# Optimization experiments

Measured on AMD Instinct MI355X. Metric: run time of the kernel, lower is better.

## Reference

```python
import jax, jax.numpy as jnp
import numpy as np

EPS = 1e-5


def conv1x1(x, w, b=None):
    # x: [B,C,H,W], w: [O,C] (1x1 conv kernel squeezed)
    y = jnp.einsum('bchw,oc->bohw', x, w)
    if b is not None:
        y = y + b[None, :, None, None]
    return y


def bn_inf(x, g, b, m, v):
    scale = g / jnp.sqrt(v + EPS)
    return (x - m[None, :, None, None]) * scale[None, :, None, None] + b[None, :, None, None]


def setup_inputs() -> dict:
    B, C, H, W = 2, 256, 80, 80
    Ck, Cv, Co = 64, 128, 256
    key = jax.random.key(0)
    ks = jax.random.split(key, 16)
    d = {}
    d['x'] = jax.random.normal(ks[0], (B, C, H, W), dtype=jnp.float32)
    d['y'] = jax.random.normal(ks[1], (B, C, H, W), dtype=jnp.float32)
    s = 1.0 / np.sqrt(C)
    d['fk_w'] = jax.random.normal(ks[2], (Ck, C), dtype=jnp.float32) * s
    d['fk_g'] = jnp.ones((Ck,), jnp.float32)
    d['fk_b'] = jnp.zeros((Ck,), jnp.float32)
    d['fk_m'] = jax.random.normal(ks[3], (Ck,), dtype=jnp.float32) * 0.1
    d['fk_v'] = jax.random.uniform(ks[4], (Ck,), minval=0.5, maxval=1.5, dtype=jnp.float32)
    d['fq_w'] = jax.random.normal(ks[5], (Ck, C), dtype=jnp.float32) * s
    d['fq_g'] = jnp.ones((Ck,), jnp.float32)
    d['fq_b'] = jnp.zeros((Ck,), jnp.float32)
    d['fq_m'] = jax.random.normal(ks[6], (Ck,), dtype=jnp.float32) * 0.1
    d['fq_v'] = jax.random.uniform(ks[7], (Ck,), minval=0.5, maxval=1.5, dtype=jnp.float32)
    d['fv_w'] = jax.random.normal(ks[8], (Cv, C), dtype=jnp.float32) * s
    d['fv_b'] = jnp.zeros((Cv,), jnp.float32)
    d['W_w'] = jax.random.normal(ks[9], (Co, Cv), dtype=jnp.float32) * (1.0 / np.sqrt(Cv))
    d['W_b'] = jnp.zeros((Co,), jnp.float32)
    d['gamma'] = jnp.array([0.5], jnp.float32)
    return d


def reference(x, y, fk_w, fk_g, fk_b, fk_m, fk_v, fq_w, fq_g, fq_b, fq_m, fq_v, fv_w, fv_b, W_w, W_b, gamma):
    B, C, H, W = x.shape
    Ck = fk_w.shape[0]
    Cv = fv_w.shape[0]
    N = H * W
    # key from x, query/value from y (1x1 conv + BN projections)
    k = bn_inf(conv1x1(x, fk_w), fk_g, fk_b, fk_m, fk_v).reshape(B, Ck, N)          # [B,Ck,N]
    q = bn_inf(conv1x1(y, fq_w), fq_g, fq_b, fq_m, fq_v).reshape(B, Ck, N)          # [B,Ck,N]
    v = conv1x1(y, fv_w, fv_b).reshape(B, Cv, N)                                     # [B,Cv,N]
    sim = jnp.einsum('bkn,bkm->bnm', q, k) * (Ck ** -0.5)                            # [B,N,N]
    sim = jax.nn.softmax(sim, axis=-1)
    ctx = jnp.einsum('bnm,bvm->bvn', sim, v).reshape(B, Cv, H, W)                    # [B,Cv,H,W]
    ctx = conv1x1(ctx, W_w, W_b)                                                     # [B,Co,H,W]
    return gamma[0] * ctx + x
```

## Files before the change

kernel.cpp:

```cpp
#include <hip/hip_runtime.h>
#include <math.h>

#define NB   2
#define CIN  256
#define NN   6400
#define CKd  64
#define CVd  128
#define COd  256

using bf16   = __bf16;
using bf16x4 = __attribute__((ext_vector_type(4))) bf16;
using bf16x8 = __attribute__((ext_vector_type(8))) bf16;
using f32x4  = __attribute__((ext_vector_type(4))) float;

__device__ __forceinline__ void lds_cp16(const void* g, void* l) {
    __builtin_amdgcn_global_load_lds((const __attribute__((address_space(1))) void*)g,
                                     (__attribute__((address_space(3))) void*)l, 16, 0, 0);
}

__global__ void prep_kernel(const float* __restrict__ fk_w, const float* __restrict__ fk_g,
                            const float* __restrict__ fk_b, const float* __restrict__ fk_m,
                            const float* __restrict__ fk_v,
                            const float* __restrict__ fq_w, const float* __restrict__ fq_g,
                            const float* __restrict__ fq_b, const float* __restrict__ fq_m,
                            const float* __restrict__ fq_v,
                            const float* __restrict__ fv_w, const float* __restrict__ fv_b,
                            const float* __restrict__ W_w,  const float* __restrict__ W_b,
                            bf16* __restrict__ wkb, bf16* __restrict__ wqb,
                            bf16* __restrict__ wvb, bf16* __restrict__ wob,
                            float* __restrict__ bias)
{
    const int idx = blockIdx.x * 256 + threadIdx.x;
    const float QS = 0.18033688011112042f;
    if (idx < 16384) {
        const int co = idx >> 8;
        const float a = fk_g[co] * rsqrtf(fk_v[co] + 1e-5f);
        wkb[idx] = (bf16)(fk_w[idx] * a);
    } else if (idx < 32768) {
        const int i = idx - 16384, co = i >> 8;
        const float a = fq_g[co] * rsqrtf(fq_v[co] + 1e-5f) * QS;
        wqb[i] = (bf16)(fq_w[i] * a);
    } else if (idx < 65536) {
        const int i = idx - 32768;
        wvb[i] = (bf16)fv_w[i];
    } else if (idx < 98304) {
        const int i = idx - 65536;
        wob[i] = (bf16)W_w[i];
    } else if (idx < 98816) {
        const int j = idx - 98304;
        if (j < 64)       { const float a = fk_g[j] * rsqrtf(fk_v[j] + 1e-5f); bias[j] = fk_b[j] - fk_m[j] * a; }
        else if (j < 128) { const int c = j - 64; const float a = fq_g[c] * rsqrtf(fq_v[c] + 1e-5f); bias[j] = (fq_b[c] - fq_m[c] * a) * QS; }
        else if (j < 256) bias[j] = fv_b[j - 128];
        else              bias[j] = W_b[j - 256];
    }
}

__launch_bounds__(256, 2)
__global__ void projkqv_kernel(const float* __restrict__ x, const float* __restrict__ y,
                               const bf16* __restrict__ wkb, const bf16* __restrict__ wqb,
                               const bf16* __restrict__ wvb, const float* __restrict__ bias,
                               bf16* __restrict__ kb, bf16* __restrict__ qb, bf16* __restrict__ vb)
{
    __shared__ __align__(16) bf16 sbuf[64 * 256];
    __shared__ __align__(16) bf16 wbuf[64 * 256];

    const int tid  = threadIdx.x;
    const int lane = tid & 63, wav = tid >> 6;
    const int l15  = lane & 15, quad = lane >> 4;
    const int b    = blockIdx.z, m = blockIdx.y;
    const int n0   = blockIdx.x * 64;

    const float* srcg = ((m == 0) ? x : y) + (size_t)b * CIN * NN;
    const bf16* wg    = (m == 0) ? wkb : (m == 1) ? wqb : (wvb + (size_t)(m - 2) * 64 * CIN);

    {
        const int r2  = lane >> 5;
        const int c32 = lane & 31;
#pragma unroll
        for (int i = 0; i < 8; ++i) {
            const int rg = wav * 16 + i * 2;
            const int r  = rg + r2;
            const int cs = c32 ^ (r & 7);
            lds_cp16(wg + (size_t)r * 256 + cs * 8, &wbuf[rg * 256]);
        }
    }

    {
        const int cb = tid >> 4;
        const int nl = (tid & 15) * 4;
#pragma unroll
        for (int p = 0; p < 16; ++p) {
            const int c = cb + p * 16;
            const float4 v = *(const float4*)(srcg + (size_t)c * NN + n0 + nl);
            const int c16 = c >> 3, ce = c & 7;
#pragma unroll
            for (int i = 0; i < 4; ++i) {
                const int n = nl + i;
                sbuf[n * 256 + ((c16 ^ (n & 7)) << 3) + ce] = (bf16)(&v.x)[i];
            }
        }
    }
    __syncthreads();

    const int key = l15 & 7;
    f32x4 acc[4];
#pragma unroll
    for (int j = 0; j < 4; ++j) acc[j] = (f32x4){0.f, 0.f, 0.f, 0.f};

    if (m < 2) {
        const int arow = wav * 16 + l15;
#pragma unroll
        for (int k4 = 0; k4 < 32; k4 += 4) {
            const bf16x8 af = *(const bf16x8*)&sbuf[arow * 256 + ((k4 + quad) ^ key) * 8];
#pragma unroll
            for (int nt = 0; nt < 4; ++nt) {
                const int brow = nt * 16 + l15;
                const bf16x8 bfw = *(const bf16x8*)&wbuf[brow * 256 + ((k4 + quad) ^ key) * 8];
                acc[nt] = __builtin_amdgcn_mfma_f32_16x16x32_bf16(af, bfw, acc[nt], 0, 0, 0);
            }
        }
        const float* bs = bias + m * 64;
        bf16* dst = (m == 0) ? kb : qb;
        const int nb = n0 + wav * 16;
#pragma unroll
        for (int nt = 0; nt < 4; ++nt) {
            const float bv = bs[nt * 16 + l15];
#pragma unroll
            for (int r = 0; r < 4; ++r) {
                const int n = nb + quad * 4 + r;
                dst[((size_t)b * NN + n) * CKd + nt * 16 + l15] = (bf16)(acc[nt][r] + bv);
            }
        }
    } else {
        const int arow = wav * 16 + l15;
#pragma unroll
        for (int k4 = 0; k4 < 32; k4 += 4) {
            const bf16x8 af = *(const bf16x8*)&wbuf[arow * 256 + ((k4 + quad) ^ key) * 8];
#pragma unroll
            for (int nt = 0; nt < 4; ++nt) {
                const int brow = nt * 16 + l15;
                const bf16x8 bfy = *(const bf16x8*)&sbuf[brow * 256 + ((k4 + quad) ^ key) * 8];
                acc[nt] = __builtin_amdgcn_mfma_f32_16x16x32_bf16(af, bfy, acc[nt], 0, 0, 0);
            }
        }
        const int cv0 = (m - 2) * 64 + wav * 16;
#pragma unroll
        for (int r = 0; r < 4; ++r) {
            const int cv = cv0 + quad * 4 + r;
            const float bv = bias[128 + cv];
#pragma unroll
            for (int nt = 0; nt < 4; ++nt)
                vb[((size_t)b * CVd + cv) * NN + n0 + nt * 16 + l15] = (bf16)(acc[nt][r] + bv);
        }
    }
}

__launch_bounds__(256, 2)
__global__ void attn_kernel(const bf16* __restrict__ qb, const bf16* __restrict__ kb,
                            const bf16* __restrict__ vb,
                            bf16* __restrict__ pO, float* __restrict__ pl, int KS)
{
    __shared__ __align__(16) bf16 kbuf[2][64 * 64];
    __shared__ __align__(16) bf16 vbuf[2][128 * 64];
    __shared__ __align__(16) bf16 p_lds[4][2][16][64];

    const int lane = threadIdx.x & 63;
    const int wav  = threadIdx.x >> 6;
    const int l15  = lane & 15;
    const int quad = lane >> 4;
    const int r8   = lane >> 3;
    const int c_src = (lane & 7) ^ r8;
    const int sw   = l15 & 7;
    const int pkey = (l15 & 7) << 1;

    const int id    = blockIdx.x;
    const int ks    = id % KS;
    const int rst   = id / KS;
    const int b     = rst & 1;
    const int qtile = rst >> 1;
    const int q0    = qtile * 256 + wav * 64;

    const bf16* qrow = qb + (size_t)b * NN * CKd;
    const bf16* krow = kb + (size_t)b * NN * CKd;
    const bf16* vrow = vb + (size_t)b * CVd * NN;

    bf16x8 qf[4][2];
#pragma unroll
    for (int qt = 0; qt < 4; ++qt)
#pragma unroll
        for (int s = 0; s < 2; ++s)
            qf[qt][s] = *(const bf16x8*)(qrow + (size_t)(q0 + qt * 16 + l15) * CKd + s * 32 + quad * 8);

    f32x4 acc[4][8];
#pragma unroll
    for (int qt = 0; qt < 4; ++qt)
#pragma unroll
        for (int cv = 0; cv < 8; ++cv) acc[qt][cv] = (f32x4){0.f, 0.f, 0.f, 0.f};
    float psum[4] = {0.f, 0.f, 0.f, 0.f};

    const int t0 = (100 * ks) / KS;
    const int nt = (100 * (ks + 1)) / KS - t0;

    auto stage = [&](int t, int bi) {
        const int key0 = t * 64;
        lds_cp16(krow + (size_t)(key0 + wav * 8 + r8) * CKd + c_src * 8,
                 &kbuf[bi][(wav * 8) * 64]);
        lds_cp16(krow + (size_t)(key0 + (wav + 4) * 8 + r8) * CKd + c_src * 8,
                 &kbuf[bi][((wav + 4) * 8) * 64]);
#pragma unroll
        for (int g4 = 0; g4 < 4; ++g4) {
            const int g = wav * 4 + g4;
            lds_cp16(vrow + (size_t)(g * 8 + r8) * NN + key0 + c_src * 8,
                     &vbuf[bi][(g * 8) * 64]);
        }
    };

    stage(t0, 0);

    for (int t = 0; t < nt; ++t) {
        __syncthreads();
        if (t + 1 < nt) stage(t0 + t + 1, (t + 1) & 1);
        const bf16* kcur = &kbuf[t & 1][0];
        const bf16* vcur = &vbuf[t & 1][0];

#pragma unroll
        for (int ph = 0; ph < 2; ++ph) {
            f32x4 s4[2][4];
#pragma unroll
            for (int kt = 0; kt < 4; ++kt) {
                const int rr = kt * 16 + l15;
                const bf16x8 kf0 = *(const bf16x8*)&kcur[rr * 64 + ((quad ^ sw) * 8)];
                const bf16x8 kf1 = *(const bf16x8*)&kcur[rr * 64 + (((4 + quad) ^ sw) * 8)];
#pragma unroll
                for (int qtl = 0; qtl < 2; ++qtl) {
                    const int qt = ph * 2 + qtl;
                    f32x4 z = (f32x4){0.f, 0.f, 0.f, 0.f};
                    z = __builtin_amdgcn_mfma_f32_16x16x32_bf16(kf0, qf[qt][0], z, 0, 0, 0);
                    z = __builtin_amdgcn_mfma_f32_16x16x32_bf16(kf1, qf[qt][1], z, 0, 0, 0);
                    s4[qtl][kt] = z;
                }
            }

#pragma unroll
            for (int qtl = 0; qtl < 2; ++qtl) {
                float ps = 0.f;
#pragma unroll
                for (int kt = 0; kt < 4; ++kt) {
                    bf16x4 pk;
#pragma unroll
                    for (int r = 0; r < 4; ++r) {
                        const float p = exp2f(s4[qtl][kt][r] - 11.541560327111707f);
                        ps += p;
                        pk[r] = (bf16)p;
                    }
                    *(bf16x4*)&p_lds[wav][qtl][l15][((kt * 4 + quad) ^ pkey) * 4] = pk;
                }
                psum[ph * 2 + qtl] += ps;
            }

#pragma unroll
            for (int sp = 0; sp < 2; ++sp) {
                const bf16x8 pf0 = *(const bf16x8*)&p_lds[wav][0][l15][((sp * 8 + quad * 2) ^ pkey) * 4];
                const bf16x8 pf1 = *(const bf16x8*)&p_lds[wav][1][l15][((sp * 8 + quad * 2) ^ pkey) * 4];
#pragma unroll
                for (int cvt = 0; cvt < 8; ++cvt) {
                    const int rr = cvt * 16 + l15;
                    const bf16x8 vf = *(const bf16x8*)&vcur[rr * 64 + (((sp * 4 + quad) ^ sw) * 8)];
                    acc[ph * 2 + 0][cvt] = __builtin_amdgcn_mfma_f32_16x16x32_bf16(vf, pf0, acc[ph * 2 + 0][cvt], 0, 0, 0);
                    acc[ph * 2 + 1][cvt] = __builtin_amdgcn_mfma_f32_16x16x32_bf16(vf, pf1, acc[ph * 2 + 1][cvt], 0, 0, 0);
                }
            }
        }
    }

    __syncthreads();
    bf16* tbuf = &p_lds[wav][0][0][0];
    const size_t pb = (size_t)ks * NB + b;
#pragma unroll
    for (int qt = 0; qt < 4; ++qt) {
        psum[qt] += __shfl_xor(psum[qt], 16);
        psum[qt] += __shfl_xor(psum[qt], 32);
#pragma unroll
        for (int cvt = 0; cvt < 8; ++cvt) {
            bf16x4 pk;
#pragma unroll
            for (int r = 0; r < 4; ++r) pk[r] = (bf16)acc[qt][cvt][r];
            const int u = (cvt * 4 + quad) ^ (l15 << 1);
            *(bf16x4*)&tbuf[l15 * 128 + u * 4] = pk;
        }
#pragma unroll
        for (int j = 0; j < 4; ++j) {
            const int row = j * 4 + (lane >> 4);
            const int g   = ((lane & 15) * 2) ^ ((row & 15) << 1);
            const bf16x8 vv = *(const bf16x8*)&tbuf[row * 128 + g * 4];
            *(bf16x8*)(pO + (pb * NN + q0 + qt * 16) * CVd + j * 512 + lane * 8) = vv;
        }
        if (quad == 0) pl[pb * NN + q0 + qt * 16 + l15] = psum[qt];
    }
}

__launch_bounds__(256, 2)
__global__ void outproj_kernel(const bf16* __restrict__ pO, const float* __restrict__ pl,
                               const bf16* __restrict__ wob, const float* __restrict__ bias,
                               const float* __restrict__ x, const float* __restrict__ gam,
                               float* __restrict__ out, int KS)
{
    __shared__ __align__(16) bf16 wbuf[256 * 128];
    __shared__ __align__(16) bf16 cbuf[32 * 128];
    __shared__ float Lrow[32];

    const int tid  = threadIdx.x;
    const int lane = tid & 63, wav = tid >> 6;
    const int l15  = lane & 15, quad = lane >> 4;
    const int b    = blockIdx.y;
    const int n0   = blockIdx.x * 32;

    {
        const int r4 = lane >> 4;
        const int c  = lane & 15;
#pragma unroll
        for (int i = 0; i < 16; ++i) {
            const int rg = wav * 64 + i * 4;
            const int r  = rg + r4;
            const int cs = c ^ (r & 7);
            lds_cp16(wob + (size_t)r * CVd + cs * 8, &wbuf[rg * 128]);
        }
    }

    const int tn = tid >> 3;
    const int tc = (tid & 7) * 16;
    float vacc[16];
#pragma unroll
    for (int i = 0; i < 16; ++i) vacc[i] = 0.f;
    for (int ksi = 0; ksi < KS; ++ksi) {
        const bf16* src = pO + ((size_t)(ksi * NB + b) * NN + n0 + tn) * CVd + tc;
#pragma unroll
        for (int j = 0; j < 2; ++j) {
            const bf16x8 v = *(const bf16x8*)(src + j * 8);
#pragma unroll
            for (int e = 0; e < 8; ++e) vacc[j * 8 + e] += (float)v[e];
        }
    }
    if (tid < 32) {
        float L = 0.f;
        for (int ksi = 0; ksi < KS; ++ksi)
            L += pl[(size_t)(ksi * NB + b) * NN + n0 + tid];
        Lrow[tid] = 1.0f / L;
    }
    __syncthreads();
    {
        const float rL = Lrow[tn];
#pragma unroll
        for (int j = 0; j < 2; ++j) {
            bf16x8 o;
#pragma unroll
            for (int e = 0; e < 8; ++e) o[e] = (bf16)(vacc[j * 8 + e] * rL);
            const int c = (tid & 7) * 2 + j;
            *(bf16x8*)&cbuf[tn * 128 + ((c ^ (tn & 7)) * 8)] = o;
        }
    }
    __syncthreads();

    f32x4 acc[4][2];
#pragma unroll
    for (int i = 0; i < 4; ++i)
#pragma unroll
        for (int j = 0; j < 2; ++j) acc[i][j] = (f32x4){0.f, 0.f, 0.f, 0.f};

#pragma unroll
    for (int kk = 0; kk < 4; ++kk) {
#pragma unroll
        for (int cot = 0; cot < 4; ++cot) {
            const int arow = wav * 64 + cot * 16 + l15;
            const bf16x8 af = *(const bf16x8*)&wbuf[arow * 128 + (((kk * 4 + quad) ^ (arow & 7)) * 8)];
#pragma unroll
            for (int nt = 0; nt < 2; ++nt) {
                const int brow = nt * 16 + l15;
                const bf16x8 bfc = *(const bf16x8*)&cbuf[brow * 128 + (((kk * 4 + quad) ^ (brow & 7)) * 8)];
                acc[cot][nt] = __builtin_amdgcn_mfma_f32_16x16x32_bf16(af, bfc, acc[cot][nt], 0, 0, 0);
            }
        }
    }

    const float gm = gam[0];
#pragma unroll
    for (int cot = 0; cot < 4; ++cot) {
#pragma unroll
        for (int r = 0; r < 4; ++r) {
            const int co = wav * 64 + cot * 16 + quad * 4 + r;
            const float bv = bias[256 + co];
#pragma unroll
            for (int nt = 0; nt < 2; ++nt) {
                const int n = n0 + nt * 16 + l15;
                const size_t a = ((size_t)b * COd + co) * NN + n;
                out[a] = gm * (acc[cot][nt][r] + bv) + x[a];
            }
        }
    }
}

extern "C" void kernel_launch(void* const* d_in, const int* in_sizes, int n_in,
                              void* d_out, int out_size, void* d_ws, size_t ws_size,
                              hipStream_t stream)
{
    const float* x     = (const float*)d_in[0];
    const float* y     = (const float*)d_in[1];
    const float* fk_w  = (const float*)d_in[2];
    const float* fk_g  = (const float*)d_in[3];
    const float* fk_b  = (const float*)d_in[4];
    const float* fk_m  = (const float*)d_in[5];
    const float* fk_v  = (const float*)d_in[6];
    const float* fq_w  = (const float*)d_in[7];
    const float* fq_g  = (const float*)d_in[8];
    const float* fq_b  = (const float*)d_in[9];
    const float* fq_m  = (const float*)d_in[10];
    const float* fq_v  = (const float*)d_in[11];
    const float* fv_w  = (const float*)d_in[12];
    const float* fv_b  = (const float*)d_in[13];
    const float* W_w   = (const float*)d_in[14];
    const float* W_b   = (const float*)d_in[15];
    const float* gamma = (const float*)d_in[16];
    float* out = (float*)d_out;

    char* ws = (char*)d_ws;
    size_t off = 0;
    auto carve = [&](size_t bytes) -> char* {
        char* p = ws + off;
        off = (off + bytes + 255) & ~(size_t)255;
        return p;
    };

    bf16*  kb   = (bf16*)carve((size_t)NB * NN * CKd * 2);
    bf16*  qbuf = (bf16*)carve((size_t)NB * NN * CKd * 2);
    bf16*  vb   = (bf16*)carve((size_t)NB * CVd * NN * 2);
    bf16*  wkb  = (bf16*)carve((size_t)CKd * CIN * 2);
    bf16*  wqb  = (bf16*)carve((size_t)CKd * CIN * 2);
    bf16*  wvb  = (bf16*)carve((size_t)CVd * CIN * 2);
    bf16*  wob  = (bf16*)carve((size_t)COd * CVd * 2);
    float* bias = (float*)carve(512 * 4);

    const size_t region = ws_size - off;
    const size_t per_ks = (size_t)NB * NN * CVd * 2 + (size_t)NB * NN * 4 + 512;
    int KS = 1;
    {
        const int cand[6] = {10, 8, 5, 4, 2, 1};
        for (int i = 0; i < 6; ++i)
            if ((size_t)cand[i] * per_ks <= region) { KS = cand[i]; break; }
    }
    bf16*  pO = (bf16*)carve((size_t)KS * NB * NN * CVd * 2);
    float* pl = (float*)carve((size_t)KS * NB * NN * 4);

    const dim3 blk(256);
    prep_kernel<<<386, blk, 0, stream>>>(fk_w, fk_g, fk_b, fk_m, fk_v,
                                         fq_w, fq_g, fq_b, fq_m, fq_v,
                                         fv_w, fv_b, W_w, W_b,
                                         wkb, wqb, wvb, wob, bias);
    projkqv_kernel<<<dim3(100, 4, NB), blk, 0, stream>>>(x, y, wkb, wqb, wvb, bias, kb, qbuf, vb);
    attn_kernel<<<dim3(25 * NB * KS), blk, 0, stream>>>(qbuf, kb, vb, pO, pl, KS);
    outproj_kernel<<<dim3(200, NB), blk, 0, stream>>>(pO, pl, wob, bias, x, gamma, out, KS);
}
```

Baseline: 173.7 us.

## Software-pipeline QK^T and PV phases in attention loop; vectorize bf16 staging stores

The attention inner loop now computes the second half's QK^T scores before issuing the first half's PV MFMAs, then runs the second half's exp and PV. This lets MFMA work overlap with the exp/ALU and LDS traffic instead of running each phase serially. P fragments are loaded into registers before the PV loop. Separately, the projection kernel's input staging packs 8 channels into one bf16x8 LDS store instead of scalar bf16 stores. The reordering raises register pressure, which could reduce occupancy or cause spills.

```diff
diff --git a/kernel.cpp b/kernel.cpp
--- a/kernel.cpp
+++ b/kernel.cpp
@@ -86,17 +86,22 @@
     }
 
     {
-        const int cb = tid >> 4;
         const int nl = (tid & 15) * 4;
-#pragma unroll
-        for (int p = 0; p < 16; ++p) {
-            const int c = cb + p * 16;
-            const float4 v = *(const float4*)(srcg + (size_t)c * NN + n0 + nl);
-            const int c16 = c >> 3, ce = c & 7;
+        const int cq = tid >> 4;
+#pragma unroll
+        for (int g = 0; g < 2; ++g) {
+            const int cb = (cq + g * 16) * 8;
+            float4 v[8];
+#pragma unroll
+            for (int e = 0; e < 8; ++e)
+                v[e] = *(const float4*)(srcg + (size_t)(cb + e) * NN + n0 + nl);
 #pragma unroll
             for (int i = 0; i < 4; ++i) {
                 const int n = nl + i;
-                sbuf[n * 256 + ((c16 ^ (n & 7)) << 3) + ce] = (bf16)(&v.x)[i];
+                bf16x8 pk;
+#pragma unroll
+                for (int e = 0; e < 8; ++e) pk[e] = (bf16)(&v[e].x)[i];
+                *(bf16x8*)&sbuf[n * 256 + (((cb >> 3) ^ (n & 7)) * 8)] = pk;
             }
         }
     }
@@ -223,53 +228,104 @@
         const bf16* kcur = &kbuf[t & 1][0];
         const bf16* vcur = &vbuf[t & 1][0];
 
-#pragma unroll
-        for (int ph = 0; ph < 2; ++ph) {
-            f32x4 s4[2][4];
+        f32x4 s4a[2][4];
+#pragma unroll
+        for (int kt = 0; kt < 4; ++kt) {
+            const int rr = kt * 16 + l15;
+            const bf16x8 kf0 = *(const bf16x8*)&kcur[rr * 64 + ((quad ^ sw) * 8)];
+            const bf16x8 kf1 = *(const bf16x8*)&kcur[rr * 64 + (((4 + quad) ^ sw) * 8)];
+#pragma unroll
+            for (int qtl = 0; qtl < 2; ++qtl) {
+                f32x4 z = (f32x4){0.f, 0.f, 0.f, 0.f};
+                z = __builtin_amdgcn_mfma_f32_16x16x32_bf16(kf0, qf[qtl][0], z, 0, 0, 0);
+                z = __builtin_amdgcn_mfma_f32_16x16x32_bf16(kf1, qf[qtl][1], z, 0, 0, 0);
+                s4a[qtl][kt] = z;
+            }
+        }
+
+#pragma unroll
+        for (int qtl = 0; qtl < 2; ++qtl) {
+            float ps = 0.f;
 #pragma unroll
             for (int kt = 0; kt < 4; ++kt) {
-                const int rr = kt * 16 + l15;
-                const bf16x8 kf0 = *(const bf16x8*)&kcur[rr * 64 + ((quad ^ sw) * 8)];
-                const bf16x8 kf1 = *(const bf16x8*)&kcur[rr * 64 + (((4 + quad) ^ sw) * 8)];
-#pragma unroll
-                for (int qtl = 0; qtl < 2; ++qtl) {
-                    const int qt = ph * 2 + qtl;
-                    f32x4 z = (f32x4){0.f, 0.f, 0.f, 0.f};
-                    z = __builtin_amdgcn_mfma_f32_16x16x32_bf16(kf0, qf[qt][0], z, 0, 0, 0);
-                    z = __builtin_amdgcn_mfma_f32_16x16x32_bf16(kf1, qf[qt][1], z, 0, 0, 0);
-                    s4[qtl][kt] = z;
+                bf16x4 pk;
+#pragma unroll
+                for (int r = 0; r < 4; ++r) {
+                    const float p = exp2f(s4a[qtl][kt][r] - 11.541560327111707f);
+                    ps += p;
+                    pk[r] = (bf16)p;
                 }
-            }
-
+                *(bf16x4*)&p_lds[wav][qtl][l15][((kt * 4 + quad) ^ pkey) * 4] = pk;
+            }
+            psum[qtl] += ps;
+        }
+
+        f32x4 s4b[2][4];
+#pragma unroll
+        for (int kt = 0; kt < 4; ++kt) {
+            const int rr = kt * 16 + l15;
+            const bf16x8 kf0 = *(const bf16x8*)&kcur[rr * 64 + ((quad ^ sw) * 8)];
+            const bf16x8 kf1 = *(const bf16x8*)&kcur[rr * 64 + (((4 + quad) ^ sw) * 8)];
 #pragma unroll
             for (int qtl = 0; qtl < 2; ++qtl) {
-                float ps = 0.f;
-#pragma unroll
-                for (int kt = 0; kt < 4; ++kt) {
-                    bf16x4 pk;
-#pragma unroll
-                    for (int r = 0; r < 4; ++r) {
-                        const float p = exp2f(s4[qtl][kt][r] - 11.541560327111707f);
-                        ps += p;
-                        pk[r] = (bf16)p;
-                    }
-                    *(bf16x4*)&p_lds[wav][qtl][l15][((kt * 4 + quad) ^ pkey) * 4] = pk;
-                }
-                psum[ph * 2 + qtl] += ps;
-            }
-
-#pragma unroll
-            for (int sp = 0; sp < 2; ++sp) {
-                const bf16x8 pf0 = *(const bf16x8*)&p_lds[wav][0][l15][((sp * 8 + quad * 2) ^ pkey) * 4];
-                const bf16x8 pf1 = *(const bf16x8*)&p_lds[wav][1][l15][((sp * 8 + quad * 2) ^ pkey) * 4];
+                f32x4 z = (f32x4){0.f, 0.f, 0.f, 0.f};
+                z = __builtin_amdgcn_mfma_f32_16x16x32_bf16(kf0, qf[2 + qtl][0], z, 0, 0, 0);
+                z = __builtin_amdgcn_mfma_f32_16x16x32_bf16(kf1, qf[2 + qtl][1], z, 0, 0, 0);
+                s4b[qtl][kt] = z;
+            }
+        }
+
+        {
+            bf16x8 pf[2][2];
+#pragma unroll
+            for (int qtl = 0; qtl < 2; ++qtl)
+#pragma unroll
+                for (int sp = 0; sp < 2; ++sp)
+                    pf[qtl][sp] = *(const bf16x8*)&p_lds[wav][qtl][l15][((sp * 8 + quad * 2) ^ pkey) * 4];
+#pragma unroll
+            for (int sp = 0; sp < 2; ++sp)
 #pragma unroll
                 for (int cvt = 0; cvt < 8; ++cvt) {
                     const int rr = cvt * 16 + l15;
                     const bf16x8 vf = *(const bf16x8*)&vcur[rr * 64 + (((sp * 4 + quad) ^ sw) * 8)];
-                    acc[ph * 2 + 0][cvt] = __builtin_amdgcn_mfma_f32_16x16x32_bf16(vf, pf0, acc[ph * 2 + 0][cvt], 0, 0, 0);
-                    acc[ph * 2 + 1][cvt] = __builtin_amdgcn_mfma_f32_16x16x32_bf16(vf, pf1, acc[ph * 2 + 1][cvt], 0, 0, 0);
+                    acc[0][cvt] = __builtin_amdgcn_mfma_f32_16x16x32_bf16(vf, pf[0][sp], acc[0][cvt], 0, 0, 0);
+                    acc[1][cvt] = __builtin_amdgcn_mfma_f32_16x16x32_bf16(vf, pf[1][sp], acc[1][cvt], 0, 0, 0);
                 }
-            }
+        }
+
+#pragma unroll
+        for (int qtl = 0; qtl < 2; ++qtl) {
+            float ps = 0.f;
+#pragma unroll
+            for (int kt = 0; kt < 4; ++kt) {
+                bf16x4 pk;
+#pragma unroll
+                for (int r = 0; r < 4; ++r) {
+                    const float p = exp2f(s4b[qtl][kt][r] - 11.541560327111707f);
+                    ps += p;
+                    pk[r] = (bf16)p;
+                }
+                *(bf16x4*)&p_lds[wav][qtl][l15][((kt * 4 + quad) ^ pkey) * 4] = pk;
+            }
+            psum[2 + qtl] += ps;
+        }
+
+        {
+            bf16x8 pf[2][2];
+#pragma unroll
+            for (int qtl = 0; qtl < 2; ++qtl)
+#pragma unroll
+                for (int sp = 0; sp < 2; ++sp)
+                    pf[qtl][sp] = *(const bf16x8*)&p_lds[wav][qtl][l15][((sp * 8 + quad * 2) ^ pkey) * 4];
+#pragma unroll
+            for (int sp = 0; sp < 2; ++sp)
+#pragma unroll
+                for (int cvt = 0; cvt < 8; ++cvt) {
+                    const int rr = cvt * 16 + l15;
+                    const bf16x8 vf = *(const bf16x8*)&vcur[rr * 64 + (((sp * 4 + quad) ^ sw) * 8)];
+                    acc[2][cvt] = __builtin_amdgcn_mfma_f32_16x16x32_bf16(vf, pf[0][sp], acc[2][cvt], 0, 0, 0);
+                    acc[3][cvt] = __builtin_amdgcn_mfma_f32_16x16x32_bf16(vf, pf[1][sp], acc[3][cvt], 0, 0, 0);
+                }
         }
     }
 
```

New measurement: 171.3 us. About the same (-1.4%).
